# Optimization experiments

Hardware: AMD Instinct MI355X
Metric: run time of the kernel (lower is better)

Reference implementation:

```python
import jax, jax.numpy as jnp
import numpy as np

H = 8          # num_heads
DK = 128       # head_k_dim = 2048*0.5/8
DV = 256       # head_v_dim = 2048*1.0/8
CHUNK = 64     # chunk length of chunk_gla
GLN = 16.0     # gate_logit_normalizer
EPS = 1e-5     # norm_eps


def setup_inputs() -> dict:
    key = jax.random.key(0)
    k1, k2, k3, k4, k5 = jax.random.split(key, 5)
    B, T, D = 4, 2048, 2048
    Kdim, Vdim, R = 1024, 2048, 16
    return {
        "segment": jax.random.normal(k1, (B, T, D), jnp.float32),
        "norm_w": jnp.ones((D,), jnp.float32),
        "Wk": jax.random.normal(k2, (D, Kdim), jnp.float32) * 0.02,
        "Wv": jax.random.normal(k3, (D, Vdim), jnp.float32) * 0.02,
        "Wg1": jax.random.normal(k4, (D, R), jnp.float32) * 0.02,
        "Wg2": jax.random.normal(k5, (R, Kdim), jnp.float32) * 0.02,
        "bg2": jnp.zeros((Kdim,), jnp.float32),
        "initial_state": jnp.zeros((B, H, DK, DV), jnp.float32),
    }


def _gla_final_state(segment, norm_w, Wk, Wv, Wg1, Wg2, bg2, initial_state):
    B, T, D = segment.shape
    # RMSNorm
    x = segment * jax.lax.rsqrt(jnp.mean(segment * segment, axis=-1, keepdims=True) + EPS)
    x = x * norm_w
    # projections (q_proj does not affect the returned state; omitted)
    k = (x @ Wk).reshape(B, T, H, DK)
    v = (x @ Wv).reshape(B, T, H, DV)
    gk = jax.nn.log_sigmoid((x @ Wg1) @ Wg2 + bg2).reshape(B, T, H, DK) / GLN

    NC = T // CHUNK
    # [NC, B, H, C, d] time-chunked, chunk-major for scan
    kc = k.reshape(B, NC, CHUNK, H, DK).transpose(1, 0, 3, 2, 4)
    vc = v.reshape(B, NC, CHUNK, H, DV).transpose(1, 0, 3, 2, 4)
    gc = gk.reshape(B, NC, CHUNK, H, DK).transpose(1, 0, 3, 2, 4)

    b = jnp.cumsum(gc, axis=3)                       # inclusive intra-chunk log-decay
    b_last = b[..., -1:, :]                          # [NC,B,H,1,DK]
    decay_k = jnp.exp(b_last - b)                    # decay from step t to chunk end
    chunk_decay = jnp.exp(b[..., -1, :])             # [NC,B,H,DK] decay of carried state
    # per-chunk outer-product accumulation: sum_t (k_t * decay) v_t^T
    kv = jnp.einsum('nbhck,nbhcv->nbhkv', kc * decay_k, vc)

    def step(S, inp):
        d, u = inp
        return S * d[..., None] + u, None

    S, _ = jax.lax.scan(step, initial_state, (chunk_decay, kv))
    return S


def reference(segment, norm_w, Wk, Wv, Wg1, Wg2, bg2, initial_state):
    return _gla_final_state(segment, norm_w, Wk, Wv, Wg1, Wg2, bg2, initial_state)
```

## Files before the change

kernel.cpp:

```cpp
#include <hip/hip_runtime.h>
#include <math.h>

#define Hh 8
#define DKc 128
#define DVc 256
#define CHUNKc 64
#define GLNf 16.0f
#define EPSf 1e-5f

#define Bb 4
#define Tt 2048
#define Dd 2048
#define KDIM 1024
#define VDIM 2048
#define Mrows 8192
#define NCHUNK 32
#define NBH 32

typedef short bf16x8 __attribute__((ext_vector_type(8)));
typedef float f32x4 __attribute__((ext_vector_type(4)));
typedef ushort ushort8v __attribute__((ext_vector_type(8)));

__device__ inline ushort f2bf(float f) {
  unsigned u = __float_as_uint(f);
  unsigned r = (u + 0x7fffu + ((u >> 16) & 1u)) >> 16;
  return (ushort)r;
}
__device__ inline float bf2f(ushort u) {
  return __uint_as_float(((unsigned)u) << 16);
}
__device__ inline float logsig(float g) {
  return fminf(g, 0.f) - __logf(1.f + __expf(-fabsf(g)));
}

__global__ __launch_bounds__(256) void rmsnorm_kernel(const float* __restrict__ seg,
                                                      const float* __restrict__ norm_w,
                                                      ushort* __restrict__ xb) {
  int row = blockIdx.x;
  int t = threadIdx.x;
  const float4* p = (const float4*)(seg + (size_t)row * Dd);
  float4 a = p[t];
  float4 b = p[t + 256];
  float ss = a.x * a.x + a.y * a.y + a.z * a.z + a.w * a.w +
             b.x * b.x + b.y * b.y + b.z * b.z + b.w * b.w;
#pragma unroll
  for (int off = 32; off > 0; off >>= 1) ss += __shfl_down(ss, off);
  __shared__ float red[4];
  if ((t & 63) == 0) red[t >> 6] = ss;
  __syncthreads();
  float tot = red[0] + red[1] + red[2] + red[3];
  float scale = rsqrtf(tot * (1.0f / (float)Dd) + EPSf);
  const float4* w4 = (const float4*)norm_w;
  float4 wa = w4[t], wb = w4[t + 256];
  ushort4 oa, ob;
  oa.x = f2bf(a.x * scale * wa.x);
  oa.y = f2bf(a.y * scale * wa.y);
  oa.z = f2bf(a.z * scale * wa.z);
  oa.w = f2bf(a.w * scale * wa.w);
  ob.x = f2bf(b.x * scale * wb.x);
  ob.y = f2bf(b.y * scale * wb.y);
  ob.z = f2bf(b.z * scale * wb.z);
  ob.w = f2bf(b.w * scale * wb.w);
  ushort4* o4 = (ushort4*)(xb + (size_t)row * Dd);
  o4[t] = oa;
  o4[t + 256] = ob;
}

__global__ __launch_bounds__(256) void transpose_all_kernel(const float* __restrict__ Wv,
                                                            const float* __restrict__ Wk,
                                                            const float* __restrict__ Wg1,
                                                            ushort* __restrict__ Wall) {
  const int K = 2048;
  __shared__ float tile[32][33];
  int k0 = blockIdx.x * 32;
  int n0 = blockIdx.y * 32;
  const float* src;
  int N, stride, nb;
  if (n0 < 2048) {
    src = Wv; N = 2048; stride = 2048; nb = n0;
  } else if (n0 < 3072) {
    src = Wk; N = 1024; stride = 1024; nb = n0 - 2048;
  } else {
    src = Wg1; N = 16; stride = 16; nb = n0 - 3072;
  }
  int tx = threadIdx.x & 31;
  int ty = threadIdx.x >> 5;
#pragma unroll
  for (int i = 0; i < 32; i += 8) {
    int k = k0 + ty + i;
    int n = nb + tx;
    tile[ty + i][tx] = (n < N) ? src[(size_t)k * stride + n] : 0.0f;
  }
  __syncthreads();
#pragma unroll
  for (int i = 0; i < 32; i += 8) {
    Wall[(size_t)(n0 + ty + i) * K + k0 + tx] = f2bf(tile[tx][ty + i]);
  }
}

__global__ __launch_bounds__(256) void transpose_x_kernel(const ushort* __restrict__ xb,
                                                          ushort* __restrict__ xT) {
  __shared__ ushort tile[32][34];
  int b = blockIdx.z;
  int t0 = blockIdx.x * 32;
  int d0 = blockIdx.y * 32;
  int tx = threadIdx.x & 31;
  int ty = threadIdx.x >> 5;
#pragma unroll
  for (int i = 0; i < 32; i += 8)
    tile[ty + i][tx] = xb[((size_t)b * Tt + t0 + ty + i) * Dd + d0 + tx];
  __syncthreads();
#pragma unroll
  for (int i = 0; i < 32; i += 8)
    xT[((size_t)b * Dd + d0 + ty + i) * Tt + t0 + tx] = tile[tx][ty + i];
}

__global__ __launch_bounds__(256) void gemm_kg_kernel(const ushort* __restrict__ A,
                                                      const ushort* __restrict__ Wallk,
                                                      ushort* __restrict__ kT,
                                                      float* __restrict__ g1) {
  __shared__ __align__(16) ushort As[128 * 32];
  __shared__ __align__(16) ushort Bs[128 * 32];
  int bm = blockIdx.x;
  int bn = blockIdx.y;
  int wave = threadIdx.x >> 6;
  int lane = threadIdx.x & 63;
  int wm = wave >> 1, wn = wave & 1;
  int lrow = lane & 15;
  int quad = lane >> 4;
  int rowInChunk = lane >> 2;
  int kElem = (lane & 3) * 8;

  f32x4 acc[4][4] = {};
  for (int kk = 0; kk < Dd; kk += 32) {
#pragma unroll
    for (int r = 0; r < 2; ++r) {
      int chunk = wave * 2 + r;
      int arow = chunk * 16 + rowInChunk;
      const ushort* ga = A + ((size_t)(bm * 128 + arow)) * Dd + kk + kElem;
      const ushort* gb = Wallk + ((size_t)(bn * 128 + arow)) * Dd + kk + kElem;
      __builtin_amdgcn_global_load_lds((__attribute__((address_space(1))) void*)ga,
                                       (__attribute__((address_space(3))) void*)(As + chunk * 512),
                                       16, 0, 0);
      __builtin_amdgcn_global_load_lds((__attribute__((address_space(1))) void*)gb,
                                       (__attribute__((address_space(3))) void*)(Bs + chunk * 512),
                                       16, 0, 0);
    }
    __syncthreads();
    bf16x8 af[4], bfr[4];
#pragma unroll
    for (int i = 0; i < 4; ++i) af[i] = *(const bf16x8*)(As + (wm * 64 + i * 16 + lrow) * 32 + quad * 8);
#pragma unroll
    for (int j = 0; j < 4; ++j) bfr[j] = *(const bf16x8*)(Bs + (wn * 64 + j * 16 + lrow) * 32 + quad * 8);
#pragma unroll
    for (int i = 0; i < 4; ++i)
#pragma unroll
      for (int j = 0; j < 4; ++j)
        acc[i][j] = __builtin_amdgcn_mfma_f32_16x16x32_bf16(af[i], bfr[j], acc[i][j], 0, 0, 0);
    __syncthreads();
  }

#pragma unroll
  for (int i = 0; i < 4; ++i) {
    int m0 = bm * 128 + wm * 64 + i * 16 + quad * 4;
    int b = m0 >> 11, tloc = m0 & 2047;
#pragma unroll
    for (int j = 0; j < 4; ++j) {
      int col = bn * 128 + wn * 64 + j * 16 + lrow;
      if (bn < 8) {
        int h = col >> 7, kd = col & 127;
        ushort4 o;
        o.x = f2bf(acc[i][j][0]);
        o.y = f2bf(acc[i][j][1]);
        o.z = f2bf(acc[i][j][2]);
        o.w = f2bf(acc[i][j][3]);
        *(ushort4*)(kT + ((size_t)((b * 8 + h) * 128 + kd)) * 2048 + tloc) = o;
      } else {
        int cg = col - 1024;
#pragma unroll
        for (int rg = 0; rg < 4; ++rg)
          g1[(size_t)(m0 + rg) * 128 + cg] = acc[i][j][rg];
      }
    }
  }
}

__global__ __launch_bounds__(256) void gemm_y_kernel(const ushort* __restrict__ kwT,
                                                     const ushort* __restrict__ xT,
                                                     ushort* __restrict__ Y) {
  __shared__ __align__(16) ushort As[128 * 32];
  __shared__ __align__(16) ushort Bs[128 * 32];
  int bn = blockIdx.x;
  int bh = blockIdx.y;
  int b = bh >> 3;
  const ushort* A = kwT + (size_t)bh * DKc * Tt;
  const ushort* B = xT + (size_t)b * Dd * Tt;
  int wave = threadIdx.x >> 6;
  int lane = threadIdx.x & 63;
  int wm = wave >> 1, wn = wave & 1;
  int lrow = lane & 15;
  int quad = lane >> 4;
  int rowInChunk = lane >> 2;
  int kElem = (lane & 3) * 8;

  f32x4 acc[4][4] = {};
  for (int kk = 0; kk < Tt; kk += 32) {
#pragma unroll
    for (int r = 0; r < 2; ++r) {
      int chunk = wave * 2 + r;
      int arow = chunk * 16 + rowInChunk;
      const ushort* ga = A + (size_t)arow * Tt + kk + kElem;
      const ushort* gb = B + ((size_t)(bn * 128 + arow)) * Tt + kk + kElem;
      __builtin_amdgcn_global_load_lds((__attribute__((address_space(1))) void*)ga,
                                       (__attribute__((address_space(3))) void*)(As + chunk * 512),
                                       16, 0, 0);
      __builtin_amdgcn_global_load_lds((__attribute__((address_space(1))) void*)gb,
                                       (__attribute__((address_space(3))) void*)(Bs + chunk * 512),
                                       16, 0, 0);
    }
    __syncthreads();
    bf16x8 af[4], bfr[4];
#pragma unroll
    for (int i = 0; i < 4; ++i) af[i] = *(const bf16x8*)(As + (wm * 64 + i * 16 + lrow) * 32 + quad * 8);
#pragma unroll
    for (int j = 0; j < 4; ++j) bfr[j] = *(const bf16x8*)(Bs + (wn * 64 + j * 16 + lrow) * 32 + quad * 8);
#pragma unroll
    for (int i = 0; i < 4; ++i)
#pragma unroll
      for (int j = 0; j < 4; ++j)
        acc[i][j] = __builtin_amdgcn_mfma_f32_16x16x32_bf16(af[i], bfr[j], acc[i][j], 0, 0, 0);
    __syncthreads();
  }

#pragma unroll
  for (int i = 0; i < 4; ++i) {
    int row0 = wm * 64 + i * 16 + quad * 4;
#pragma unroll
    for (int j = 0; j < 4; ++j) {
      int col = bn * 128 + wn * 64 + j * 16 + lrow;
#pragma unroll
      for (int rg = 0; rg < 4; ++rg)
        Y[((size_t)bh * DKc + row0 + rg) * Dd + col] = f2bf(acc[i][j][rg]);
    }
  }
}

__global__ __launch_bounds__(256) void gemm_out_kernel(const ushort* __restrict__ Y,
                                                       const ushort* __restrict__ WvT,
                                                       const float* __restrict__ eBtot,
                                                       const float* __restrict__ S0,
                                                       float* __restrict__ out) {
  __shared__ __align__(16) ushort As[128 * 32];
  __shared__ __align__(16) ushort Bs[128 * 32];
  int bn = blockIdx.x;
  int bh = blockIdx.y;
  int h = bh & 7;
  const ushort* A = Y + (size_t)bh * DKc * Dd;
  const ushort* B = WvT + (size_t)(h * DVc + bn * 128) * Dd;
  int wave = threadIdx.x >> 6;
  int lane = threadIdx.x & 63;
  int wm = wave >> 1, wn = wave & 1;
  int lrow = lane & 15;
  int quad = lane >> 4;
  int rowInChunk = lane >> 2;
  int kElem = (lane & 3) * 8;

  f32x4 acc[4][4] = {};
  for (int kk = 0; kk < Dd; kk += 32) {
#pragma unroll
    for (int r = 0; r < 2; ++r) {
      int chunk = wave * 2 + r;
      int arow = chunk * 16 + rowInChunk;
      const ushort* ga = A + (size_t)arow * Dd + kk + kElem;
      const ushort* gb = B + (size_t)arow * Dd + kk + kElem;
      __builtin_amdgcn_global_load_lds((__attribute__((address_space(1))) void*)ga,
                                       (__attribute__((address_space(3))) void*)(As + chunk * 512),
                                       16, 0, 0);
      __builtin_amdgcn_global_load_lds((__attribute__((address_space(1))) void*)gb,
                                       (__attribute__((address_space(3))) void*)(Bs + chunk * 512),
                                       16, 0, 0);
    }
    __syncthreads();
    bf16x8 af[4], bfr[4];
#pragma unroll
    for (int i = 0; i < 4; ++i) af[i] = *(const bf16x8*)(As + (wm * 64 + i * 16 + lrow) * 32 + quad * 8);
#pragma unroll
    for (int j = 0; j < 4; ++j) bfr[j] = *(const bf16x8*)(Bs + (wn * 64 + j * 16 + lrow) * 32 + quad * 8);
#pragma unroll
    for (int i = 0; i < 4; ++i)
#pragma unroll
      for (int j = 0; j < 4; ++j)
        acc[i][j] = __builtin_amdgcn_mfma_f32_16x16x32_bf16(af[i], bfr[j], acc[i][j], 0, 0, 0);
    __syncthreads();
  }

  size_t base = (size_t)bh * DKc * DVc;
#pragma unroll
  for (int i = 0; i < 4; ++i) {
    int row0 = wm * 64 + i * 16 + quad * 4;
#pragma unroll
    for (int j = 0; j < 4; ++j) {
      int col = bn * 128 + wn * 64 + j * 16 + lrow;
#pragma unroll
      for (int rg = 0; rg < 4; ++rg) {
        int r = row0 + rg;
        out[base + (size_t)r * DVc + col] =
            S0[base + (size_t)r * DVc + col] * eBtot[bh * DKc + r] + acc[i][j][rg];
      }
    }
  }
}

__global__ __launch_bounds__(128) void chunksum_kernel(const float* __restrict__ g1,
                                                       const float* __restrict__ Wg2,
                                                       const float* __restrict__ bg2,
                                                       float* __restrict__ L) {
  int n = blockIdx.x, bh = blockIdx.y;
  int b = bh >> 3, h = bh & 7;
  int t = threadIdx.x;
  int kdg = h * DKc + t;
  int trow = b * Tt + n * CHUNKc;
  __shared__ float g1s[CHUNKc * 16];
#pragma unroll
  for (int i = 0; i < 8; ++i) {
    int flat = i * 128 + t;
    int c = flat >> 4, r = flat & 15;
    g1s[flat] = g1[(size_t)(trow + c) * 128 + r];
  }
  float wc[16];
#pragma unroll
  for (int r = 0; r < 16; ++r) wc[r] = Wg2[r * KDIM + kdg];
  float bias = bg2[kdg];
  __syncthreads();
  float sum = 0.f;
  for (int c = 0; c < CHUNKc; ++c) {
    float dot = bias;
#pragma unroll
    for (int r = 0; r < 16; ++r) dot = fmaf(g1s[c * 16 + r], wc[r], dot);
    sum += logsig(dot) * (1.0f / GLNf);
  }
  L[((size_t)bh * NCHUNK + n) * DKc + t] = sum;
}

__global__ __launch_bounds__(128) void weight_kernel(const float* __restrict__ g1,
                                                     const float* __restrict__ Wg2,
                                                     const float* __restrict__ bg2,
                                                     const float* __restrict__ L,
                                                     ushort* __restrict__ kwT,
                                                     float* __restrict__ eBtot) {
  int n = blockIdx.x, bh = blockIdx.y;
  int b = bh >> 3, h = bh & 7;
  int t = threadIdx.x;
  int kdg = h * DKc + t;
  int trow = b * Tt + n * CHUNKc;
  __shared__ float g1s[CHUNKc * 16];
#pragma unroll
  for (int i = 0; i < 8; ++i) {
    int flat = i * 128 + t;
    int c = flat >> 4, r = flat & 15;
    g1s[flat] = g1[(size_t)(trow + c) * 128 + r];
  }
  float wc[16];
#pragma unroll
  for (int r = 0; r < 16; ++r) wc[r] = Wg2[r * KDIM + kdg];
  float bias = bg2[kdg];

  float suffix = 0.f, Ln = 0.f, Btot = 0.f;
#pragma unroll
  for (int m = 0; m < NCHUNK; ++m) {
    float Lm = L[((size_t)bh * NCHUNK + m) * DKc + t];
    if (m > n) suffix += Lm;
    if (m == n) Ln = Lm;
    Btot += Lm;
  }
  if (n == 0) eBtot[bh * DKc + t] = __expf(Btot);
  __syncthreads();

  float run = 0.f;
  size_t obase = ((size_t)bh * DKc + t) * (size_t)Tt + (size_t)n * CHUNKc;
  for (int cg = 0; cg < 8; ++cg) {
    ushort8v kw8;
    ushort8v k8 = *(const ushort8v*)(kwT + obase + cg * 8);
#pragma unroll
    for (int j = 0; j < 8; ++j) {
      int c = cg * 8 + j;
      float dot = bias;
#pragma unroll
      for (int r = 0; r < 16; ++r) dot = fmaf(g1s[c * 16 + r], wc[r], dot);
      run += logsig(dot) * (1.0f / GLNf);
      float w = __expf(suffix + Ln - run);
      kw8[j] = f2bf(bf2f(k8[j]) * w);
    }
    *(ushort8v*)(kwT + obase + cg * 8) = kw8;
  }
}

extern "C" void kernel_launch(void* const* d_in, const int* in_sizes, int n_in,
                              void* d_out, int out_size, void* d_ws, size_t ws_size,
                              hipStream_t stream) {
  const float* seg = (const float*)d_in[0];
  const float* norm_w = (const float*)d_in[1];
  const float* Wk = (const float*)d_in[2];
  const float* Wv = (const float*)d_in[3];
  const float* Wg1 = (const float*)d_in[4];
  const float* Wg2 = (const float*)d_in[5];
  const float* bg2 = (const float*)d_in[6];
  const float* S0 = (const float*)d_in[7];
  float* out = (float*)d_out;
  char* ws = (char*)d_ws;

  char* regA = ws;
  char* regB = ws + (size_t)32 * 1024 * 1024;
  char* regD = ws + (size_t)64 * 1024 * 1024;
  char* regC = ws + (size_t)80 * 1024 * 1024;
  float* Lbuf = (float*)(regC + 13107200);
  float* eBtot = (float*)(regC + 13107200 + 524288);

  ushort* xb = (ushort*)regA;
  ushort* Y = (ushort*)regA;
  ushort* xT = (ushort*)regB;
  ushort* kwT = (ushort*)regD;
  ushort* Wall = (ushort*)regC;
  ushort* Wallk = Wall + (size_t)2048 * 2048;
  float* g1buf = (float*)d_out;

  rmsnorm_kernel<<<Mrows, 256, 0, stream>>>(seg, norm_w, xb);
  transpose_all_kernel<<<dim3(64, 100), 256, 0, stream>>>(Wv, Wk, Wg1, Wall);
  transpose_x_kernel<<<dim3(64, 64, 4), 256, 0, stream>>>(xb, xT);
  gemm_kg_kernel<<<dim3(64, 9), 256, 0, stream>>>(xb, Wallk, kwT, g1buf);
  chunksum_kernel<<<dim3(NCHUNK, NBH), 128, 0, stream>>>(g1buf, Wg2, bg2, Lbuf);
  weight_kernel<<<dim3(NCHUNK, NBH), 128, 0, stream>>>(g1buf, Wg2, bg2, Lbuf, kwT, eBtot);
  gemm_y_kernel<<<dim3(16, NBH), 256, 0, stream>>>(kwT, xT, Y);
  gemm_out_kernel<<<dim3(2, NBH), 256, 0, stream>>>(Y, Wall, eBtot, S0, out);
}
```

Before: 360.0 us.

## Split-K the final state GEMM, vectorize x transpose, remap kg grid

The final gemm_out GEMM, which launched only 64 blocks over a K of 2048, becomes a 4-way split-K kernel writing fp32 partials into workspace. A new reduce kernel sums the partials and applies the decayed initial state. The x transpose now uses 64x64 tiles with 4-wide vector loads and stores, and the kg GEMM grid is flattened so consecutive blocks share the same A row tile. This adds an extra launch and extra partial-sum traffic in exchange for better CU occupancy on the last GEMM.

```diff
diff --git a/kernel.cpp b/kernel.cpp
--- a/kernel.cpp
+++ b/kernel.cpp
@@ -100,19 +100,34 @@
 
 __global__ __launch_bounds__(256) void transpose_x_kernel(const ushort* __restrict__ xb,
                                                           ushort* __restrict__ xT) {
-  __shared__ ushort tile[32][34];
+  __shared__ ushort tile[64 * 65];
   int b = blockIdx.z;
-  int t0 = blockIdx.x * 32;
-  int d0 = blockIdx.y * 32;
-  int tx = threadIdx.x & 31;
-  int ty = threadIdx.x >> 5;
-#pragma unroll
-  for (int i = 0; i < 32; i += 8)
-    tile[ty + i][tx] = xb[((size_t)b * Tt + t0 + ty + i) * Dd + d0 + tx];
+  int t0 = blockIdx.x * 64;
+  int d0 = blockIdx.y * 64;
+  int tx = threadIdx.x & 15;
+  int ty = threadIdx.x >> 4;
+#pragma unroll
+  for (int i = 0; i < 4; ++i) {
+    int t = i * 16 + ty;
+    ushort4 v = *(const ushort4*)(xb + ((size_t)b * Tt + t0 + t) * Dd + d0 + tx * 4);
+    tile[t * 65 + tx * 4 + 0] = v.x;
+    tile[t * 65 + tx * 4 + 1] = v.y;
+    tile[t * 65 + tx * 4 + 2] = v.z;
+    tile[t * 65 + tx * 4 + 3] = v.w;
+  }
   __syncthreads();
-#pragma unroll
-  for (int i = 0; i < 32; i += 8)
-    xT[((size_t)b * Dd + d0 + ty + i) * Tt + t0 + tx] = tile[tx][ty + i];
+  int tw = threadIdx.x & 15;
+  int dw = threadIdx.x >> 4;
+#pragma unroll
+  for (int j = 0; j < 4; ++j) {
+    int d = j * 16 + dw;
+    ushort4 o;
+    o.x = tile[(tw * 4 + 0) * 65 + d];
+    o.y = tile[(tw * 4 + 1) * 65 + d];
+    o.z = tile[(tw * 4 + 2) * 65 + d];
+    o.w = tile[(tw * 4 + 3) * 65 + d];
+    *(ushort4*)(xT + ((size_t)b * Dd + d0 + d) * Tt + t0 + tw * 4) = o;
+  }
 }
 
 __global__ __launch_bounds__(256) void gemm_kg_kernel(const ushort* __restrict__ A,
@@ -121,8 +136,8 @@
                                                       float* __restrict__ g1) {
   __shared__ __align__(16) ushort As[128 * 32];
   __shared__ __align__(16) ushort Bs[128 * 32];
-  int bm = blockIdx.x;
-  int bn = blockIdx.y;
+  int bm = blockIdx.x / 9;
+  int bn = blockIdx.x % 9;
   int wave = threadIdx.x >> 6;
   int lane = threadIdx.x & 63;
   int wm = wave >> 1, wn = wave & 1;
@@ -245,15 +260,14 @@
   }
 }
 
-__global__ __launch_bounds__(256) void gemm_out_kernel(const ushort* __restrict__ Y,
-                                                       const ushort* __restrict__ WvT,
-                                                       const float* __restrict__ eBtot,
-                                                       const float* __restrict__ S0,
-                                                       float* __restrict__ out) {
+__global__ __launch_bounds__(256) void gemm_out_sk_kernel(const ushort* __restrict__ Y,
+                                                          const ushort* __restrict__ WvT,
+                                                          float* __restrict__ Spart) {
   __shared__ __align__(16) ushort As[128 * 32];
   __shared__ __align__(16) ushort Bs[128 * 32];
   int bn = blockIdx.x;
   int bh = blockIdx.y;
+  int ks = blockIdx.z;
   int h = bh & 7;
   const ushort* A = Y + (size_t)bh * DKc * Dd;
   const ushort* B = WvT + (size_t)(h * DVc + bn * 128) * Dd;
@@ -266,7 +280,8 @@
   int kElem = (lane & 3) * 8;
 
   f32x4 acc[4][4] = {};
-  for (int kk = 0; kk < Dd; kk += 32) {
+  int kk0 = ks * 512;
+  for (int kk = kk0; kk < kk0 + 512; kk += 32) {
 #pragma unroll
     for (int r = 0; r < 2; ++r) {
       int chunk = wave * 2 + r;
@@ -294,7 +309,7 @@
     __syncthreads();
   }
 
-  size_t base = (size_t)bh * DKc * DVc;
+  float* Sp = Spart + ((size_t)ks * NBH + bh) * (DKc * DVc);
 #pragma unroll
   for (int i = 0; i < 4; ++i) {
     int row0 = wm * 64 + i * 16 + quad * 4;
@@ -302,13 +317,32 @@
     for (int j = 0; j < 4; ++j) {
       int col = bn * 128 + wn * 64 + j * 16 + lrow;
 #pragma unroll
-      for (int rg = 0; rg < 4; ++rg) {
-        int r = row0 + rg;
-        out[base + (size_t)r * DVc + col] =
-            S0[base + (size_t)r * DVc + col] * eBtot[bh * DKc + r] + acc[i][j][rg];
-      }
-    }
-  }
+      for (int rg = 0; rg < 4; ++rg)
+        Sp[(size_t)(row0 + rg) * DVc + col] = acc[i][j][rg];
+    }
+  }
+}
+
+__global__ __launch_bounds__(256) void reduce_kernel(const float* __restrict__ Spart,
+                                                     const float* __restrict__ eBtot,
+                                                     const float* __restrict__ S0,
+                                                     float* __restrict__ out) {
+  int i4 = blockIdx.x * 256 + threadIdx.x;
+  int idx = i4 * 4;
+  int bh = idx >> 15;
+  int kd = (idx >> 8) & 127;
+  float e = eBtot[bh * DKc + kd];
+  float4 a = ((const float4*)S0)[i4];
+  float4 p0 = ((const float4*)Spart)[i4];
+  float4 p1 = ((const float4*)Spart)[i4 + 262144];
+  float4 p2 = ((const float4*)Spart)[i4 + 524288];
+  float4 p3 = ((const float4*)Spart)[i4 + 786432];
+  float4 r;
+  r.x = a.x * e + p0.x + p1.x + p2.x + p3.x;
+  r.y = a.y * e + p0.y + p1.y + p2.y + p3.y;
+  r.z = a.z * e + p0.z + p1.z + p2.z + p3.z;
+  r.w = a.w * e + p0.w + p1.w + p2.w + p3.w;
+  ((float4*)out)[i4] = r;
 }
 
 __global__ __launch_bounds__(128) void chunksum_kernel(const float* __restrict__ g1,
@@ -420,16 +454,18 @@
   ushort* Y = (ushort*)regA;
   ushort* xT = (ushort*)regB;
   ushort* kwT = (ushort*)regD;
+  float* Spart = (float*)regD;
   ushort* Wall = (ushort*)regC;
   ushort* Wallk = Wall + (size_t)2048 * 2048;
   float* g1buf = (float*)d_out;
 
   rmsnorm_kernel<<<Mrows, 256, 0, stream>>>(seg, norm_w, xb);
   transpose_all_kernel<<<dim3(64, 100), 256, 0, stream>>>(Wv, Wk, Wg1, Wall);
-  transpose_x_kernel<<<dim3(64, 64, 4), 256, 0, stream>>>(xb, xT);
-  gemm_kg_kernel<<<dim3(64, 9), 256, 0, stream>>>(xb, Wallk, kwT, g1buf);
+  transpose_x_kernel<<<dim3(32, 32, 4), 256, 0, stream>>>(xb, xT);
+  gemm_kg_kernel<<<576, 256, 0, stream>>>(xb, Wallk, kwT, g1buf);
   chunksum_kernel<<<dim3(NCHUNK, NBH), 128, 0, stream>>>(g1buf, Wg2, bg2, Lbuf);
   weight_kernel<<<dim3(NCHUNK, NBH), 128, 0, stream>>>(g1buf, Wg2, bg2, Lbuf, kwT, eBtot);
   gemm_y_kernel<<<dim3(16, NBH), 256, 0, stream>>>(kwT, xT, Y);
-  gemm_out_kernel<<<dim3(2, NBH), 256, 0, stream>>>(Y, Wall, eBtot, S0, out);
-}
+  gemm_out_sk_kernel<<<dim3(2, NBH, 4), 256, 0, stream>>>(Y, Wall, Spart);
+  reduce_kernel<<<1024, 256, 0, stream>>>(Spart, eBtot, S0, out);
+}
```

Result: faster. 348.1 us (-3.3%).
